# Optimization experiments

Measured on AMD Instinct MI355X. Metric: run time of the kernel, lower is better.

## Reference

```python
import jax, jax.numpy as jnp
import numpy as np

B, S, D = 2, 2048, 1024
H, E = 16, 64  # n_head, d_head


def setup_inputs() -> dict:
    key = jax.random.key(0)
    ks = jax.random.split(key, 5)
    scale = 0.02
    return {
        "x": jax.random.normal(ks[0], (B, S, D), dtype=jnp.float32),
        "Wq": jax.random.normal(ks[1], (H, D, E), dtype=jnp.float32) * scale,
        "Wk": jax.random.normal(ks[2], (H, D, E), dtype=jnp.float32) * scale,
        "Wv": jax.random.normal(ks[3], (H, D, E), dtype=jnp.float32) * scale,
        "Wproj": jax.random.normal(ks[4], (D, D), dtype=jnp.float32) * scale,
    }


def reference(x, Wq, Wk, Wv, Wproj):
    # Batched equivalent of the per-head Python loop.
    q = jnp.einsum("bsd,hde->bhse", x, Wq)  # [B,H,S,E]
    k = jnp.einsum("bsd,hde->bhse", x, Wk)
    v = jnp.einsum("bsd,hde->bhse", x, Wv)
    scale = 1.0 / jnp.sqrt(jnp.asarray(E, dtype=x.dtype))
    scores = jnp.einsum("bhse,bhte->bhst", q, k) * scale  # [B,H,S,S]
    causal = jnp.tril(jnp.ones((S, S), dtype=bool))
    scores = jnp.where(causal, scores, jnp.asarray(-jnp.inf, dtype=scores.dtype))
    attn = jax.nn.softmax(scores, axis=-1)
    out = jnp.einsum("bhst,bhte->bhse", attn, v)  # [B,H,S,E]
    # concat heads along last dim (head h -> contiguous slice), then proj
    out = out.transpose(0, 2, 1, 3).reshape(B, S, H * E)
    return out @ Wproj.T  # nn.Linear: y = x W^T
```

## Files before the change

kernel.cpp:

```cpp
#include <hip/hip_runtime.h>
#include <hip/hip_bf16.h>

typedef __attribute__((ext_vector_type(8))) short short8;
typedef __attribute__((ext_vector_type(4))) short s16x4;
typedef __attribute__((ext_vector_type(4))) float f32x4;
typedef __hip_bfloat16 bf16;

#define NB 2
#define NS 2048
#define ND 1024
#define NH 16
#define NE 64

#define QSCALE 0.1803368867f

#define ASYNC16(g, l) __builtin_amdgcn_global_load_lds( \
    (const __attribute__((address_space(1))) void*)(g), \
    (__attribute__((address_space(3))) void*)(l), 16, 0, 0)

__device__ __forceinline__ unsigned short bf16b(float x) {
  __hip_bfloat16 h = __float2bfloat16(x);
  unsigned short u;
  __builtin_memcpy(&u, &h, 2);
  return u;
}

__global__ __launch_bounds__(256) void prep_all(const float* __restrict__ x,
                                                bf16* __restrict__ xb,
                                                const float* __restrict__ wp,
                                                bf16* __restrict__ wpb,
                                                const float* __restrict__ Wq,
                                                const float* __restrict__ Wk,
                                                const float* __restrict__ Wv,
                                                bf16* __restrict__ WT) {
  const int bid = blockIdx.x;
  const int tid = threadIdx.x;
  if (bid < 2560) {
    const float* src;
    bf16* dst;
    int i;
    if (bid < 2048) { src = x;  dst = xb;  i = (bid * 256 + tid) * 8; }
    else            { src = wp; dst = wpb; i = ((bid - 2048) * 256 + tid) * 8; }
    const float4 a = *(const float4*)(src + i);
    const float4 b = *(const float4*)(src + i + 4);
    *(ushort4*)(dst + i)     = make_ushort4(bf16b(a.x), bf16b(a.y), bf16b(a.z), bf16b(a.w));
    *(ushort4*)(dst + i + 4) = make_ushort4(bf16b(b.x), bf16b(b.y), bf16b(b.z), bf16b(b.w));
    return;
  }
  const int tb = bid - 2560;
  const int w = tb >> 8;
  const int xx = tb & 255;
  const float* W = (w == 0) ? Wq : ((w == 1) ? Wk : Wv);
  const int h = xx >> 4, kt = xx & 15;
  __shared__ bf16 tile[64][65];
#pragma unroll
  for (int i = 0; i < 16; ++i) {
    const int idx = i * 256 + tid, kl = idx >> 6, e = idx & 63;
    tile[kl][e] = __float2bfloat16(W[((size_t)h * ND + kt * 64 + kl) * NE + e]);
  }
  __syncthreads();
#pragma unroll
  for (int i = 0; i < 16; ++i) {
    const int idx = i * 256 + tid, el = idx >> 6, kl = idx & 63;
    WT[((size_t)w * NH * NE + h * NE + el) * ND + kt * 64 + kl] = tile[kl][el];
  }
}

__global__ __launch_bounds__(256) void qkv_gemm(const bf16* __restrict__ X,
                                                const bf16* __restrict__ WT,
                                                bf16* __restrict__ Qo,
                                                bf16* __restrict__ Ko,
                                                bf16* __restrict__ Vo) {
  const int w = blockIdx.z;
  const bf16* Bm = WT + (size_t)w * (NH * NE * ND);
  const int n0 = blockIdx.x * 128, m0 = blockIdx.y * 128;
  __shared__ __align__(16) bf16 As[2][128 * 32];
  __shared__ __align__(16) bf16 Bs[2][128 * 32];
  const int tid = threadIdx.x;
  const int lane = tid & 63, wid = tid >> 6;
  const int wm = wid >> 1, wn = wid & 1;
  const int g = lane >> 4, c = lane & 15;
  const int row4 = tid >> 2;
  const int kcs = ((tid & 3) ^ ((tid >> 2) & 3)) * 8;

  auto stage = [&](int buf, int k0) {
    ASYNC16(X + (size_t)(m0 + row4) * ND + k0 + kcs, As[buf] + wid * 512);
    ASYNC16(X + (size_t)(m0 + 64 + row4) * ND + k0 + kcs, As[buf] + 2048 + wid * 512);
    ASYNC16(Bm + (size_t)(n0 + row4) * ND + k0 + kcs, Bs[buf] + wid * 512);
    ASYNC16(Bm + (size_t)(n0 + 64 + row4) * ND + k0 + kcs, Bs[buf] + 2048 + wid * 512);
  };

  f32x4 acc[4][4] = {};
  stage(0, 0);
  __syncthreads();
  int cur = 0;
  for (int k0 = 0; k0 < ND; k0 += 32) {
    if (k0 + 32 < ND) stage(cur ^ 1, k0 + 32);
    const short* as = (const short*)As[cur];
    const short* bs = (const short*)Bs[cur];
    short8 af[4], bq[4];
#pragma unroll
    for (int i = 0; i < 4; ++i)
      af[i] = *(const short8*)&as[(wm * 64 + i * 16 + c) * 32 + ((g ^ (c & 3)) * 8)];
#pragma unroll
    for (int j = 0; j < 4; ++j)
      bq[j] = *(const short8*)&bs[(wn * 64 + j * 16 + c) * 32 + ((g ^ (c & 3)) * 8)];
    __builtin_amdgcn_s_setprio(1);
#pragma unroll
    for (int i = 0; i < 4; ++i)
#pragma unroll
      for (int j = 0; j < 4; ++j)
        acc[i][j] = __builtin_amdgcn_mfma_f32_16x16x32_bf16(af[i], bq[j], acc[i][j], 0, 0, 0);
    __builtin_amdgcn_s_setprio(0);
    __syncthreads();
    cur ^= 1;
  }
  const float osc = (w == 0) ? QSCALE : 1.0f;
#pragma unroll
  for (int i = 0; i < 4; ++i) {
    const int mg0 = m0 + wm * 64 + i * 16 + g * 4;
#pragma unroll
    for (int j = 0; j < 4; ++j) {
      const int ng = n0 + wn * 64 + j * 16 + c;
      const int h = ng >> 6, e = ng & 63;
      if (w == 2) {
        const int b = mg0 >> 11, s = mg0 & 2047;
        ushort4 pk = make_ushort4(bf16b(acc[i][j][0]), bf16b(acc[i][j][1]),
                                  bf16b(acc[i][j][2]), bf16b(acc[i][j][3]));
        *(ushort4*)&Vo[(((size_t)b * NH + h) * NE + e) * NS + s] = pk;
      } else {
        bf16* O = (w == 0) ? Qo : Ko;
#pragma unroll
        for (int r = 0; r < 4; ++r) {
          const int m = mg0 + r, b = m >> 11, s = m & 2047;
          O[(((size_t)b * NH + h) * NS + s) * NE + e] = __float2bfloat16(acc[i][j][r] * osc);
        }
      }
    }
  }
}

__global__ __launch_bounds__(256, 4) void attn_fwd(const bf16* __restrict__ Qb,
                                                   const bf16* __restrict__ Kb,
                                                   const bf16* __restrict__ Vt,
                                                   bf16* __restrict__ AO) {
  const int bh = blockIdx.x;
  const int qi = blockIdx.y;
  const int a = qi & 7, k = qi >> 3;
  const int qt = (k == 0) ? a : (k == 1) ? 31 - a : (k == 2) ? a + 8 : 23 - a;
  const int q0 = qt * 64;
  __shared__ __align__(16) bf16 Ks[2][64 * 64];
  __shared__ __align__(16) bf16 Vs[2][64 * 64];
  __shared__ __align__(16) bf16 Ps[4][16 * 64];
  const int tid = threadIdx.x, lane = tid & 63, wid = tid >> 6;
  const int g = lane >> 4, c = lane & 15;
  const int sw8 = ((tid & 7) ^ ((tid >> 3) & 7)) * 8;
  const bf16* Qg = Qb + (size_t)bh * NS * NE;
  const bf16* Kg = Kb + (size_t)bh * NS * NE;
  const bf16* Vg = Vt + (size_t)bh * NE * NS;

  short8 aq[2];
#pragma unroll
  for (int kk = 0; kk < 2; ++kk)
    aq[kk] = *(const short8*)&Qg[(size_t)(q0 + wid * 16 + c) * NE + kk * 32 + g * 8];

  const short8 bones = {0x3F80, 0x3F80, 0x3F80, 0x3F80, 0x3F80, 0x3F80, 0x3F80, 0x3F80};

  f32x4 acc_o[4] = {};
  f32x4 acc_l = {};
  float mrun = -1.0e30f;

  auto stage = [&](int buf, int t0) {
    ASYNC16(Kg + (size_t)(t0 + (tid >> 3)) * NE + sw8,      Ks[buf] + wid * 512);
    ASYNC16(Kg + (size_t)(t0 + 32 + (tid >> 3)) * NE + sw8, Ks[buf] + 2048 + wid * 512);
    ASYNC16(Vg + (size_t)(tid >> 3) * NS + t0 + sw8,        Vs[buf] + wid * 512);
    ASYNC16(Vg + (size_t)(32 + (tid >> 3)) * NS + t0 + sw8, Vs[buf] + 2048 + wid * 512);
  };

  const int nt = qt + 1;
  int cur = 0;
  stage(0, 0);
  __syncthreads();
  for (int tt = 0; tt < nt; ++tt) {
    const int t0 = tt * 64;
    if (tt + 1 < nt) stage(cur ^ 1, t0 + 64);
    const bool diag = (tt == nt - 1);
    f32x4 sacc[4] = {};
    const short* ks = (const short*)Ks[cur];
    const short* vs = (const short*)Vs[cur];
    __builtin_amdgcn_s_setprio(1);
#pragma unroll
    for (int kk = 0; kk < 2; ++kk) {
      short8 bk[4];
#pragma unroll
      for (int tn = 0; tn < 4; ++tn)
        bk[tn] = *(const short8*)&ks[(tn * 16 + c) * 64 + (((kk * 4 + g) ^ (c & 7)) * 8)];
#pragma unroll
      for (int tn = 0; tn < 4; ++tn)
        sacc[tn] = __builtin_amdgcn_mfma_f32_16x16x32_bf16(bk[tn], aq[kk], sacc[tn], 0, 0, 0);
    }
    __builtin_amdgcn_s_setprio(0);
    float mx = -1.0e30f;
#pragma unroll
    for (int tn = 0; tn < 4; ++tn) {
#pragma unroll
      for (int r = 0; r < 4; ++r) {
        float v = sacc[tn][r];
        if (diag) {
          const int tcol = t0 + tn * 16 + g * 4 + r;
          const int qrow = q0 + wid * 16 + c;
          v = (tcol <= qrow) ? v : -1.0e30f;
          sacc[tn][r] = v;
        }
        mx = fmaxf(mx, v);
      }
    }
    if (__any(mx > mrun + 8.0f)) {
      mx = fmaxf(mx, __shfl_xor(mx, 16));
      mx = fmaxf(mx, __shfl_xor(mx, 32));
      const float mnew = fmaxf(mrun, mx);
      const float alpha = __builtin_exp2f(mrun - mnew);
      mrun = mnew;
      float al[4];
#pragma unroll
      for (int r = 0; r < 4; ++r) al[r] = __shfl(alpha, g * 4 + r);
#pragma unroll
      for (int fe = 0; fe < 4; ++fe)
#pragma unroll
        for (int r = 0; r < 4; ++r) acc_o[fe][r] *= al[r];
#pragma unroll
      for (int r = 0; r < 4; ++r) acc_l[r] *= al[r];
    }
    short* psw = (short*)Ps[wid];
#pragma unroll
    for (int tn = 0; tn < 4; ++tn) {
      s16x4 pw;
#pragma unroll
      for (int r = 0; r < 4; ++r)
        pw[r] = (short)bf16b(__builtin_exp2f(sacc[tn][r] - mrun));
      const int blk = (2 * tn + (g >> 1)) ^ (c & 7);
      *(s16x4*)&psw[c * 64 + blk * 8 + (g & 1) * 4] = pw;
    }
    const short* ps = (const short*)Ps[wid];
    __builtin_amdgcn_s_setprio(1);
#pragma unroll
    for (int ks2 = 0; ks2 < 2; ++ks2) {
      short8 ap, bv[4];
      ap = *(const short8*)&ps[c * 64 + (((ks2 * 4 + g) ^ (c & 7)) * 8)];
      acc_l = __builtin_amdgcn_mfma_f32_16x16x32_bf16(ap, bones, acc_l, 0, 0, 0);
#pragma unroll
      for (int fe = 0; fe < 4; ++fe)
        bv[fe] = *(const short8*)&vs[(fe * 16 + c) * 64 + (((ks2 * 4 + g) ^ (c & 7)) * 8)];
#pragma unroll
      for (int fe = 0; fe < 4; ++fe)
        acc_o[fe] = __builtin_amdgcn_mfma_f32_16x16x32_bf16(ap, bv[fe], acc_o[fe], 0, 0, 0);
    }
    __builtin_amdgcn_s_setprio(0);
    __syncthreads();
    cur ^= 1;
  }
  const int b = bh >> 4, h = bh & 15;
#pragma unroll
  for (int fe = 0; fe < 4; ++fe)
#pragma unroll
    for (int r = 0; r < 4; ++r) {
      const int s = q0 + wid * 16 + g * 4 + r;
      const float val = acc_o[fe][r] / acc_l[r];
      AO[((size_t)b * NS + s) * ND + h * NE + fe * 16 + c] = __float2bfloat16(val);
    }
}

__global__ __launch_bounds__(256) void proj_gemm(const bf16* __restrict__ A,
                                                 const bf16* __restrict__ Wp,
                                                 float* __restrict__ Y) {
  const int n0 = blockIdx.x * 128, m0 = blockIdx.y * 128;
  __shared__ __align__(16) bf16 As[2][128 * 32];
  __shared__ __align__(16) bf16 Bs[2][128 * 32];
  const int tid = threadIdx.x;
  const int lane = tid & 63, wid = tid >> 6;
  const int wm = wid >> 1, wn = wid & 1;
  const int g = lane >> 4, c = lane & 15;
  const int row4 = tid >> 2;
  const int kcs = ((tid & 3) ^ ((tid >> 2) & 3)) * 8;

  auto stage = [&](int buf, int k0) {
    ASYNC16(A + (size_t)(m0 + row4) * ND + k0 + kcs, As[buf] + wid * 512);
    ASYNC16(A + (size_t)(m0 + 64 + row4) * ND + k0 + kcs, As[buf] + 2048 + wid * 512);
    ASYNC16(Wp + (size_t)(n0 + row4) * ND + k0 + kcs, Bs[buf] + wid * 512);
    ASYNC16(Wp + (size_t)(n0 + 64 + row4) * ND + k0 + kcs, Bs[buf] + 2048 + wid * 512);
  };

  f32x4 acc[4][4] = {};
  stage(0, 0);
  __syncthreads();
  int cur = 0;
  for (int k0 = 0; k0 < ND; k0 += 32) {
    if (k0 + 32 < ND) stage(cur ^ 1, k0 + 32);
    const short* as = (const short*)As[cur];
    const short* bs = (const short*)Bs[cur];
    short8 af[4], bq[4];
#pragma unroll
    for (int i = 0; i < 4; ++i)
      af[i] = *(const short8*)&as[(wm * 64 + i * 16 + c) * 32 + ((g ^ (c & 3)) * 8)];
#pragma unroll
    for (int j = 0; j < 4; ++j)
      bq[j] = *(const short8*)&bs[(wn * 64 + j * 16 + c) * 32 + ((g ^ (c & 3)) * 8)];
    __builtin_amdgcn_s_setprio(1);
#pragma unroll
    for (int i = 0; i < 4; ++i)
#pragma unroll
      for (int j = 0; j < 4; ++j)
        acc[i][j] = __builtin_amdgcn_mfma_f32_16x16x32_bf16(af[i], bq[j], acc[i][j], 0, 0, 0);
    __builtin_amdgcn_s_setprio(0);
    __syncthreads();
    cur ^= 1;
  }
#pragma unroll
  for (int i = 0; i < 4; ++i) {
    const int mg0 = m0 + wm * 64 + i * 16 + g * 4;
#pragma unroll
    for (int j = 0; j < 4; ++j) {
      const int ng = n0 + wn * 64 + j * 16 + c;
#pragma unroll
      for (int r = 0; r < 4; ++r)
        Y[(size_t)(mg0 + r) * ND + ng] = acc[i][j][r];
    }
  }
}

extern "C" void kernel_launch(void* const* d_in, const int* in_sizes, int n_in,
                              void* d_out, int out_size, void* d_ws, size_t ws_size,
                              hipStream_t stream) {
  const float* x  = (const float*)d_in[0];
  const float* Wq = (const float*)d_in[1];
  const float* Wk = (const float*)d_in[2];
  const float* Wv = (const float*)d_in[3];
  const float* Wp = (const float*)d_in[4];
  float* out = (float*)d_out;

  bf16* ws = (bf16*)d_ws;
  bf16* Xb  = ws;
  bf16* WT  = Xb + (size_t)NB * NS * ND;
  bf16* Wpb = WT + (size_t)3 * NH * NE * ND;
  bf16* Qb  = Wpb + (size_t)ND * ND;
  bf16* Kb  = Qb + (size_t)NB * NH * NS * NE;
  bf16* Vt  = Kb + (size_t)NB * NH * NS * NE;
  bf16* AO  = Vt + (size_t)NB * NH * NS * NE;

  hipLaunchKernelGGL(prep_all, dim3(3328), dim3(256), 0, stream,
                     x, Xb, Wp, Wpb, Wq, Wk, Wv, WT);
  hipLaunchKernelGGL(qkv_gemm, dim3(8, 32, 3), dim3(256), 0, stream, Xb, WT, Qb, Kb, Vt);
  hipLaunchKernelGGL(attn_fwd, dim3(32, 32), dim3(256), 0, stream, Qb, Kb, Vt, AO);
  hipLaunchKernelGGL(proj_gemm, dim3(8, 32), dim3(256), 0, stream, AO, Wpb, out);
}
```

Before: 107.7 us.

## Use partial vmcnt waits for true double buffering and change LDS swizzle

Replaces __syncthreads with explicit s_waitcnt vmcnt(4) plus raw s_barrier, so only the previous stage's async global-to-LDS loads are awaited while the next stage's loads stay in flight. The GEMM LDS swizzle is also changed from row&3 to (row>>2)&3 to reduce bank conflicts on the fragment reads. The hand-written waitcnt relies on the compiler not emitting other outstanding vector memory ops, which risks races or a stall if the count is wrong.

```diff
diff --git a/kernel.cpp b/kernel.cpp
--- a/kernel.cpp
+++ b/kernel.cpp
@@ -17,6 +17,8 @@
 #define ASYNC16(g, l) __builtin_amdgcn_global_load_lds( \
     (const __attribute__((address_space(1))) void*)(g), \
     (__attribute__((address_space(3))) void*)(l), 16, 0, 0)
+
+#define MEMFENCE asm volatile("" ::: "memory")
 
 __device__ __forceinline__ unsigned short bf16b(float x) {
   __hip_bfloat16 h = __float2bfloat16(x);
@@ -81,7 +83,7 @@
   const int wm = wid >> 1, wn = wid & 1;
   const int g = lane >> 4, c = lane & 15;
   const int row4 = tid >> 2;
-  const int kcs = ((tid & 3) ^ ((tid >> 2) & 3)) * 8;
+  const int kcs = ((tid & 3) ^ ((tid >> 4) & 3)) * 8;
 
   auto stage = [&](int buf, int k0) {
     ASYNC16(X + (size_t)(m0 + row4) * ND + k0 + kcs, As[buf] + wid * 512);
@@ -92,19 +94,25 @@
 
   f32x4 acc[4][4] = {};
   stage(0, 0);
-  __syncthreads();
   int cur = 0;
   for (int k0 = 0; k0 < ND; k0 += 32) {
-    if (k0 + 32 < ND) stage(cur ^ 1, k0 + 32);
+    if (k0 + 32 < ND) {
+      stage(cur ^ 1, k0 + 32);
+      asm volatile("s_waitcnt vmcnt(4)");
+    } else {
+      asm volatile("s_waitcnt vmcnt(0)");
+    }
+    __builtin_amdgcn_s_barrier();
+    MEMFENCE;
     const short* as = (const short*)As[cur];
     const short* bs = (const short*)Bs[cur];
     short8 af[4], bq[4];
 #pragma unroll
     for (int i = 0; i < 4; ++i)
-      af[i] = *(const short8*)&as[(wm * 64 + i * 16 + c) * 32 + ((g ^ (c & 3)) * 8)];
+      af[i] = *(const short8*)&as[(wm * 64 + i * 16 + c) * 32 + ((g ^ (c >> 2)) * 8)];
 #pragma unroll
     for (int j = 0; j < 4; ++j)
-      bq[j] = *(const short8*)&bs[(wn * 64 + j * 16 + c) * 32 + ((g ^ (c & 3)) * 8)];
+      bq[j] = *(const short8*)&bs[(wn * 64 + j * 16 + c) * 32 + ((g ^ (c >> 2)) * 8)];
     __builtin_amdgcn_s_setprio(1);
 #pragma unroll
     for (int i = 0; i < 4; ++i)
@@ -112,7 +120,8 @@
       for (int j = 0; j < 4; ++j)
         acc[i][j] = __builtin_amdgcn_mfma_f32_16x16x32_bf16(af[i], bq[j], acc[i][j], 0, 0, 0);
     __builtin_amdgcn_s_setprio(0);
-    __syncthreads();
+    __builtin_amdgcn_s_barrier();
+    MEMFENCE;
     cur ^= 1;
   }
   const float osc = (w == 0) ? QSCALE : 1.0f;
@@ -180,10 +189,16 @@
   const int nt = qt + 1;
   int cur = 0;
   stage(0, 0);
-  __syncthreads();
   for (int tt = 0; tt < nt; ++tt) {
     const int t0 = tt * 64;
-    if (tt + 1 < nt) stage(cur ^ 1, t0 + 64);
+    if (tt + 1 < nt) {
+      stage(cur ^ 1, t0 + 64);
+      asm volatile("s_waitcnt vmcnt(4)");
+    } else {
+      asm volatile("s_waitcnt vmcnt(0)");
+    }
+    __builtin_amdgcn_s_barrier();
+    MEMFENCE;
     const bool diag = (tt == nt - 1);
     f32x4 sacc[4] = {};
     const short* ks = (const short*)Ks[cur];
@@ -256,7 +271,8 @@
         acc_o[fe] = __builtin_amdgcn_mfma_f32_16x16x32_bf16(ap, bv[fe], acc_o[fe], 0, 0, 0);
     }
     __builtin_amdgcn_s_setprio(0);
-    __syncthreads();
+    __builtin_amdgcn_s_barrier();
+    MEMFENCE;
     cur ^= 1;
   }
   const int b = bh >> 4, h = bh & 15;
@@ -281,7 +297,7 @@
   const int wm = wid >> 1, wn = wid & 1;
   const int g = lane >> 4, c = lane & 15;
   const int row4 = tid >> 2;
-  const int kcs = ((tid & 3) ^ ((tid >> 2) & 3)) * 8;
+  const int kcs = ((tid & 3) ^ ((tid >> 4) & 3)) * 8;
 
   auto stage = [&](int buf, int k0) {
     ASYNC16(A + (size_t)(m0 + row4) * ND + k0 + kcs, As[buf] + wid * 512);
@@ -292,19 +308,25 @@
 
   f32x4 acc[4][4] = {};
   stage(0, 0);
-  __syncthreads();
   int cur = 0;
   for (int k0 = 0; k0 < ND; k0 += 32) {
-    if (k0 + 32 < ND) stage(cur ^ 1, k0 + 32);
+    if (k0 + 32 < ND) {
+      stage(cur ^ 1, k0 + 32);
+      asm volatile("s_waitcnt vmcnt(4)");
+    } else {
+      asm volatile("s_waitcnt vmcnt(0)");
+    }
+    __builtin_amdgcn_s_barrier();
+    MEMFENCE;
     const short* as = (const short*)As[cur];
     const short* bs = (const short*)Bs[cur];
     short8 af[4], bq[4];
 #pragma unroll
     for (int i = 0; i < 4; ++i)
-      af[i] = *(const short8*)&as[(wm * 64 + i * 16 + c) * 32 + ((g ^ (c & 3)) * 8)];
+      af[i] = *(const short8*)&as[(wm * 64 + i * 16 + c) * 32 + ((g ^ (c >> 2)) * 8)];
 #pragma unroll
     for (int j = 0; j < 4; ++j)
-      bq[j] = *(const short8*)&bs[(wn * 64 + j * 16 + c) * 32 + ((g ^ (c & 3)) * 8)];
+      bq[j] = *(const short8*)&bs[(wn * 64 + j * 16 + c) * 32 + ((g ^ (c >> 2)) * 8)];
     __builtin_amdgcn_s_setprio(1);
 #pragma unroll
     for (int i = 0; i < 4; ++i)
@@ -312,7 +334,8 @@
       for (int j = 0; j < 4; ++j)
         acc[i][j] = __builtin_amdgcn_mfma_f32_16x16x32_bf16(af[i], bq[j], acc[i][j], 0, 0, 0);
     __builtin_amdgcn_s_setprio(0);
-    __syncthreads();
+    __builtin_amdgcn_s_barrier();
+    MEMFENCE;
     cur ^= 1;
   }
 #pragma unroll
```

Measured after the change: 129.4 us. +20.2%, slower.
